# Performance work log

Measured on AMD Instinct MI355X. Metric: run time of the kernel, lower is better.

Reference implementation:

```python
import jax, jax.numpy as jnp
import numpy as np

D_MODEL = 1024
N_HEADS = 16


def setup_inputs() -> dict:
    key = jax.random.key(0)
    ks = jax.random.split(key, 5)
    sigma = (1.0 / D_MODEL) ** 0.5
    return {
        "x": jax.random.normal(ks[0], (4, 2048, D_MODEL), dtype=jnp.float32),
        "W_q": jax.random.normal(ks[1], (D_MODEL, D_MODEL), dtype=jnp.float32) * sigma,
        "W_k": jax.random.normal(ks[2], (D_MODEL, D_MODEL), dtype=jnp.float32) * sigma,
        "W_v": jax.random.normal(ks[3], (D_MODEL, D_MODEL), dtype=jnp.float32) * sigma,
        "W_o": jax.random.normal(ks[4], (D_MODEL, D_MODEL), dtype=jnp.float32) * sigma,
    }


def reference(x, W_q, W_k, W_v, W_o):
    b, s, d = x.shape
    h = N_HEADS
    d_h = d // h
    # Projections: original does einsum('d_out dim, ... dim -> ... d_out') == x @ W.T
    def proj(W):
        y = jnp.einsum('bsd,ed->bse', x, W)
        # ... seq (head d_h) -> ... head seq d_h
        return y.reshape(b, s, h, d_h).transpose(0, 2, 1, 3)
    Q, K, V = proj(W_q), proj(W_k), proj(W_v)
    scale = 1.0 / jnp.sqrt(jnp.asarray(d_h, dtype=x.dtype))
    scores = jnp.einsum('bhqd,bhkd->bhqk', Q, K) * scale  # [b,h,s,s]
    causal = jnp.tril(jnp.ones((s, s), dtype=bool))
    scores = jnp.where(causal, scores, -jnp.inf)
    attn = jax.nn.softmax(scores, axis=-1)
    out = jnp.einsum('bhqk,bhkd->bhqd', attn, V)  # [b,h,s,d_h]
    out = out.transpose(0, 2, 1, 3).reshape(b, s, d)
    # einsum(Temp, W_o, '... dim1, dim dim1 -> ... dim') == Temp @ W_o.T
    return jnp.einsum('bse,de->bsd', out, W_o)
```

## Files before the change

### kernel.cpp

```cpp
#include <hip/hip_runtime.h>

typedef __attribute__((ext_vector_type(8))) short s16x8;
typedef __attribute__((ext_vector_type(4))) short s16x4;
typedef __attribute__((ext_vector_type(4))) float f32x4;
typedef unsigned short u16;
typedef unsigned int u32;
typedef unsigned long long u64;

__device__ __forceinline__ u16 f2bf(float f) {
  unsigned u = __builtin_bit_cast(unsigned, f);
  return (u16)((u + 0x7fffu + ((u >> 16) & 1u)) >> 16);
}

#define QSCALE 0.18033688011112042f

__device__ __forceinline__ void gld16(const u16* g, u16* l) {
  __builtin_amdgcn_global_load_lds(
      (const __attribute__((address_space(1))) void*)g,
      (__attribute__((address_space(3))) void*)l, 16, 0, 0);
}

__device__ __forceinline__ u32 pack_trunc(float a, float b) {
  return __builtin_amdgcn_perm(__builtin_bit_cast(u32, b),
                               __builtin_bit_cast(u32, a), 0x07060302u);
}

__global__ __launch_bounds__(256)
void cvt_all(const float* __restrict__ x,  u16* __restrict__ xb,
             const float* __restrict__ w0, u16* __restrict__ w0b,
             const float* __restrict__ w1, u16* __restrict__ w1b,
             const float* __restrict__ w2, u16* __restrict__ w2b,
             const float* __restrict__ w3, u16* __restrict__ w3b)
{
  int bb = blockIdx.x;
  const float* src; u16* dst; int i;
  if (bb < 4096)      { src = x;  dst = xb;  i = bb * 256 + threadIdx.x; }
  else if (bb < 4608) { src = w0; dst = w0b; i = (bb - 4096) * 256 + threadIdx.x; }
  else if (bb < 5120) { src = w1; dst = w1b; i = (bb - 4608) * 256 + threadIdx.x; }
  else if (bb < 5632) { src = w2; dst = w2b; i = (bb - 5120) * 256 + threadIdx.x; }
  else                { src = w3; dst = w3b; i = (bb - 5632) * 256 + threadIdx.x; }
  f32x4 a = ((const f32x4*)src)[2 * i];
  f32x4 b = ((const f32x4*)src)[2 * i + 1];
  s16x8 pk;
  pk[0] = (short)f2bf(a[0]); pk[1] = (short)f2bf(a[1]);
  pk[2] = (short)f2bf(a[2]); pk[3] = (short)f2bf(a[3]);
  pk[4] = (short)f2bf(b[0]); pk[5] = (short)f2bf(b[1]);
  pk[6] = (short)f2bf(b[2]); pk[7] = (short)f2bf(b[3]);
  ((s16x8*)dst)[i] = pk;
}

template<bool OUT_QKV>
__global__ __launch_bounds__(256)
void gemm97(const u16* __restrict__ A,
            const u16* __restrict__ B0, const u16* __restrict__ B1,
            const u16* __restrict__ B2,
            u16* __restrict__ o0, u16* __restrict__ o1, u16* __restrict__ o2,
            float* __restrict__ oF)
{
  const int by = blockIdx.x;
  const int bx = blockIdx.y;
  const int bz = blockIdx.z;
  const u16* B = (bz == 0) ? B0 : ((bz == 1) ? B1 : B2);
  u16* oQ = (bz == 0) ? o0 : ((bz == 1) ? o1 : o2);

  __shared__ u16 As[128 * 32];
  __shared__ u16 Bs[128 * 32];

  const int tid  = threadIdx.x;
  const int w    = tid >> 6;
  const int lane = tid & 63;
  const int quad = lane >> 4;
  const int l15  = lane & 15;
  const int wm   = (w >> 1) * 64;
  const int wn   = (w & 1) * 64;

  const int arb  = w * 32;
  const int srow = lane >> 2;
  const int scol = (lane & 3) * 8;
  const u16* ga = A + (size_t)(by * 128 + arb + srow) * 1024 + scol;
  const u16* gb = B + (size_t)(bx * 128 + arb + srow) * 1024 + scol;
  u16* la0 = &As[arb * 32];
  u16* la1 = &As[(arb + 16) * 32];
  u16* lb0 = &Bs[arb * 32];
  u16* lb1 = &Bs[(arb + 16) * 32];

  f32x4 acc[4][4];
  #pragma unroll
  for (int i = 0; i < 4; ++i)
    #pragma unroll
    for (int j = 0; j < 4; ++j)
      acc[i][j] = (f32x4){0.f, 0.f, 0.f, 0.f};

  for (int k0 = 0; k0 < 1024; k0 += 32) {
    gld16(ga + k0,               la0);
    gld16(ga + k0 + 16 * 1024,   la1);
    gld16(gb + k0,               lb0);
    gld16(gb + k0 + 16 * 1024,   lb1);
    __syncthreads();

    s16x8 af[4], bf[4];
    #pragma unroll
    for (int i = 0; i < 4; ++i)
      af[i] = *(const s16x8*)&As[(wm + i * 16 + l15) * 32 + quad * 8];
    #pragma unroll
    for (int i = 0; i < 4; ++i)
      bf[i] = *(const s16x8*)&Bs[(wn + i * 16 + l15) * 32 + quad * 8];
    #pragma unroll
    for (int mt = 0; mt < 4; ++mt)
      #pragma unroll
      for (int nt = 0; nt < 4; ++nt)
        acc[mt][nt] = __builtin_amdgcn_mfma_f32_16x16x32_bf16(
            af[mt], bf[nt], acc[mt][nt], 0, 0, 0);
    __syncthreads();
  }

  #pragma unroll
  for (int mt = 0; mt < 4; ++mt)
    #pragma unroll
    for (int nt = 0; nt < 4; ++nt)
      #pragma unroll
      for (int r = 0; r < 4; ++r) {
        const int row = by * 128 + wm + mt * 16 + quad * 4 + r;
        const int col = bx * 128 + wn + nt * 16 + l15;
        float v = acc[mt][nt][r];
        if (OUT_QKV) {
          const int b = row >> 11, s = row & 2047, hh = col >> 6, d = col & 63;
          if (bz == 2) {
            oQ[(size_t)(b * 16 + hh) * 131072 + d * 2048 + s] = f2bf(v);
          } else {
            if (bz == 0) v *= QSCALE;
            oQ[(size_t)(b * 16 + hh) * 131072 + s * 64 + d] = f2bf(v);
          }
        } else {
          oF[(size_t)row * 1024 + col] = v;
        }
      }
}

#define ATTN_STEP(t, Pw, qtt)                                                  \
  do {                                                                         \
    f32x4 S[4];                                                                \
    _Pragma("unroll")                                                          \
    for (int nt = 0; nt < 4; ++nt) {                                           \
      s16x8 b0 = *(const s16x8*)&Ks[(nt * 16 + l15) * 32 + quad * 8];          \
      s16x8 b1 = *(const s16x8*)&Ks[2048 + (nt * 16 + l15) * 32 + quad * 8];   \
      f32x4 z = (f32x4){0.f, 0.f, 0.f, 0.f};                                   \
      z = __builtin_amdgcn_mfma_f32_16x16x32_bf16(aq[t][0], b0, z, 0, 0, 0);   \
      z = __builtin_amdgcn_mfma_f32_16x16x32_bf16(aq[t][1], b1, z, 0, 0, 0);   \
      S[nt] = z;                                                               \
    }                                                                          \
    if (j == (qtt)) {                                                          \
      _Pragma("unroll")                                                        \
      for (int nt = 0; nt < 4; ++nt)                                           \
        _Pragma("unroll")                                                      \
        for (int r = 0; r < 4; ++r) {                                          \
          const int kg = 4 * l15 + nt;                                         \
          const int qg = w * 16 + quad * 4 + r;                                \
          if (kg > qg) S[nt][r] = -1e30f;                                      \
        }                                                                      \
    }                                                                          \
    _Pragma("unroll")                                                          \
    for (int r = 0; r < 4; ++r) {                                              \
      float rm = fmaxf(fmaxf(S[0][r], S[1][r]), fmaxf(S[2][r], S[3][r]));      \
      _Pragma("unroll")                                                        \
      for (int off = 1; off < 16; off <<= 1)                                   \
        rm = fmaxf(rm, __shfl_xor(rm, off, 64));                               \
      const float mold = mi[t][r];                                             \
      const float mnew = fmaxf(mold, rm);                                      \
      const float alpha = __builtin_amdgcn_exp2f(mold - mnew);                 \
      mi[t][r] = mnew;                                                         \
      const float p0 = __builtin_amdgcn_exp2f(S[0][r] - mnew);                 \
      const float p1 = __builtin_amdgcn_exp2f(S[1][r] - mnew);                 \
      const float p2 = __builtin_amdgcn_exp2f(S[2][r] - mnew);                 \
      const float p3 = __builtin_amdgcn_exp2f(S[3][r] - mnew);                 \
      liacc[t][r] *= alpha;                                                    \
      _Pragma("unroll")                                                        \
      for (int dt = 0; dt < 4; ++dt) O[t][dt][r] *= alpha;                     \
      const u64 pk = (u64)pack_trunc(p0, p1) |                                 \
                     ((u64)pack_trunc(p2, p3) << 32);                          \
      *(u64*)&(Pw)[(quad * 4 + r) * 68 + 4 * l15] = pk;                        \
    }                                                                          \
    s16x8 a0 = *(const s16x8*)&(Pw)[l15 * 68 + quad * 8];                      \
    s16x8 a1 = *(const s16x8*)&(Pw)[l15 * 68 + 32 + quad * 8];                 \
    liacc[t] = __builtin_amdgcn_mfma_f32_16x16x32_bf16(a0, ones, liacc[t], 0, 0, 0); \
    liacc[t] = __builtin_amdgcn_mfma_f32_16x16x32_bf16(a1, ones, liacc[t], 0, 0, 0); \
    _Pragma("unroll")                                                          \
    for (int dt = 0; dt < 4; ++dt) {                                           \
      s16x8 b0 = *(const s16x8*)&Vt[(dt * 16 + l15) * 32 + quad * 8];          \
      s16x8 b1 = *(const s16x8*)&Vt[2048 + (dt * 16 + l15) * 32 + quad * 8];   \
      O[t][dt] = __builtin_amdgcn_mfma_f32_16x16x32_bf16(a0, b0, O[t][dt], 0, 0, 0); \
      O[t][dt] = __builtin_amdgcn_mfma_f32_16x16x32_bf16(a1, b1, O[t][dt], 0, 0, 0); \
    }                                                                          \
  } while (0)

__global__ __launch_bounds__(256, 4)
void attn_kernel(const u16* __restrict__ Qg, const u16* __restrict__ Kg,
                 const u16* __restrict__ VTg, u16* __restrict__ out)
{
  const int pi = blockIdx.x;
  const int bh = blockIdx.y;
  const int b = bh >> 4, h = bh & 15;
  const int qt0 = 31 - pi;
  const int qt1 = pi;

  __shared__ u16 Qs[128 * 68];
  __shared__ u16 Ks[2 * 64 * 32];
  __shared__ u16 Vt[2 * 64 * 32];

  const int tid = threadIdx.x;
  const int w = tid >> 6, lane = tid & 63, quad = lane >> 4, l15 = lane & 15;
  const size_t base = (size_t)bh * 131072;

  {
    const int col = (tid & 7) * 8;
    #pragma unroll
    for (int p = 0; p < 4; ++p) {
      const int row = (tid >> 3) + p * 32;
      const int gq = (row < 64) ? (qt0 * 64 + row) : (qt1 * 64 + (row - 64));
      *(s16x8*)&Qs[row * 68 + col] =
          *(const s16x8*)(Qg + base + (size_t)gq * 64 + col);
    }
  }
  __syncthreads();

  s16x8 aq[2][2];
  #pragma unroll
  for (int t = 0; t < 2; ++t)
    #pragma unroll
    for (int ks = 0; ks < 2; ++ks)
      aq[t][ks] = *(const s16x8*)&Qs[(t * 64 + w * 16 + l15) * 68 + ks * 32 + quad * 8];

  u16* Pw0 = &Qs[(w * 16) * 68];
  u16* Pw1 = &Qs[(64 + w * 16) * 68];

  s16x8 ones;
  #pragma unroll
  for (int e = 0; e < 8; ++e) ones[e] = (short)0x3F80;

  f32x4 O[2][4], liacc[2];
  float mi[2][4];
  #pragma unroll
  for (int t = 0; t < 2; ++t) {
    #pragma unroll
    for (int dt = 0; dt < 4; ++dt) O[t][dt] = (f32x4){0.f, 0.f, 0.f, 0.f};
    liacc[t] = (f32x4){0.f, 0.f, 0.f, 0.f};
    #pragma unroll
    for (int r = 0; r < 4; ++r) mi[t][r] = -1e30f;
  }

  const int kkey   = (lane >> 2) * 4 + w;
  const int vd     = w * 16 + (lane >> 2);
  const int chunk  = (lane & 3) * 8;
  const u16* gk = Kg  + base + (size_t)kkey * 64 + chunk;
  const u16* gv = VTg + base + (size_t)vd * 2048 + chunk;
  u16* lk0 = &Ks[w * 16 * 32];
  u16* lk1 = &Ks[2048 + w * 16 * 32];
  u16* lv0 = &Vt[w * 16 * 32];
  u16* lv1 = &Vt[2048 + w * 16 * 32];

  for (int j = 0; j <= qt0; ++j) {
    const size_t koff = (size_t)j * 4096;
    const size_t voff = (size_t)j * 64;
    gld16(gk + koff,      lk0);
    gld16(gk + koff + 32, lk1);
    gld16(gv + voff,      lv0);
    gld16(gv + voff + 32, lv1);
    __syncthreads();

    ATTN_STEP(0, Pw0, qt0);
    if (j <= qt1) ATTN_STEP(1, Pw1, qt1);
    __syncthreads();
  }

  #pragma unroll
  for (int t = 0; t < 2; ++t) {
    const int qtt = t ? qt1 : qt0;
    #pragma unroll
    for (int r = 0; r < 4; ++r) {
      const float inv = __builtin_amdgcn_rcpf(liacc[t][r]);
      const int sq = qtt * 64 + w * 16 + quad * 4 + r;
      #pragma unroll
      for (int dt = 0; dt < 4; ++dt)
        out[(size_t)(b * 2048 + sq) * 1024 + h * 64 + dt * 16 + l15] =
            f2bf(O[t][dt][r] * inv);
    }
  }
}

extern "C" void kernel_launch(void* const* d_in, const int* in_sizes, int n_in,
                              void* d_out, int out_size, void* d_ws, size_t ws_size,
                              hipStream_t stream) {
  (void)in_sizes; (void)n_in; (void)out_size; (void)ws_size;
  const float* x  = (const float*)d_in[0];
  const float* Wq = (const float*)d_in[1];
  const float* Wk = (const float*)d_in[2];
  const float* Wv = (const float*)d_in[3];
  const float* Wo = (const float*)d_in[4];
  float* out = (float*)d_out;

  u16* W16 = (u16*)d_ws;
  u16* xb  = W16;
  u16* AO  = W16;
  u16* Qb  = W16 + 8388608;
  u16* Kb  = W16 + 16777216;
  u16* VT  = W16 + 25165824;
  u16* Wqb = W16 + 33554432;
  u16* Wkb = Wqb + 1048576;
  u16* Wvb = Wkb + 1048576;
  u16* Wob = Wvb + 1048576;

  dim3 blk(256);
  cvt_all<<<dim3(6144), blk, 0, stream>>>(x, xb, Wq, Wqb, Wk, Wkb,
                                          Wv, Wvb, Wo, Wob);
  gemm97<true ><<<dim3(64, 8, 3), blk, 0, stream>>>(
      xb, Wqb, Wkb, Wvb, Qb, Kb, VT, nullptr);
  attn_kernel<<<dim3(16, 64), blk, 0, stream>>>(Qb, Kb, VT, AO);
  gemm97<false><<<dim3(64, 8, 1), blk, 0, stream>>>(
      AO, Wob, Wob, Wob, nullptr, nullptr, nullptr, out);
}
```

Before: 301.8 us.

## Pre-tile K/V in LDS-ready layout and double-buffer K loads in attention

The QKV GEMM epilogue now writes K and V^T directly in the per-64-key tile layout the attention kernel copies into LDS, packing V stores into 64-bit writes. The attention kernel then streams contiguous 8 KB tiles, double-buffers K so the next tile is prefetched during the current step, and overlaps the V load with the QK^T/softmax phase. Q fragments are read straight from global memory and the LDS Q staging is dropped. This removes strided gathers and one barrier per step, at the cost of a tighter sync ordering around the single V buffer and P scratch, which is now shared by both query tiles.

```diff
diff --git a/kernel.cpp b/kernel.cpp
--- a/kernel.cpp
+++ b/kernel.cpp
@@ -117,27 +117,42 @@
   #pragma unroll
   for (int mt = 0; mt < 4; ++mt)
     #pragma unroll
-    for (int nt = 0; nt < 4; ++nt)
-      #pragma unroll
-      for (int r = 0; r < 4; ++r) {
-        const int row = by * 128 + wm + mt * 16 + quad * 4 + r;
-        const int col = bx * 128 + wn + nt * 16 + l15;
-        float v = acc[mt][nt][r];
-        if (OUT_QKV) {
-          const int b = row >> 11, s = row & 2047, hh = col >> 6, d = col & 63;
-          if (bz == 2) {
-            oQ[(size_t)(b * 16 + hh) * 131072 + d * 2048 + s] = f2bf(v);
-          } else {
-            if (bz == 0) v *= QSCALE;
-            oQ[(size_t)(b * 16 + hh) * 131072 + s * 64 + d] = f2bf(v);
+    for (int nt = 0; nt < 4; ++nt) {
+      const int row0 = by * 128 + wm + mt * 16 + quad * 4;
+      const int col  = bx * 128 + wn + nt * 16 + l15;
+      if (OUT_QKV) {
+        const int b = row0 >> 11, s0 = row0 & 2047;
+        const int hh = col >> 6, d = col & 63;
+        const size_t hb = (size_t)(b * 16 + hh) * 131072;
+        if (bz == 2) {
+          const int tile = s0 >> 6, key0 = s0 & 63;
+          const u64 pk = (u64)f2bf(acc[mt][nt][0])
+                       | ((u64)f2bf(acc[mt][nt][1]) << 16)
+                       | ((u64)f2bf(acc[mt][nt][2]) << 32)
+                       | ((u64)f2bf(acc[mt][nt][3]) << 48);
+          *(u64*)&oQ[hb + tile * 4096 + (key0 >> 5) * 2048 + d * 32 + (key0 & 31)] = pk;
+        } else if (bz == 1) {
+          #pragma unroll
+          for (int r = 0; r < 4; ++r) {
+            const int s = s0 + r, tile = s >> 6, key = s & 63;
+            const int slot = (key & 3) * 16 + (key >> 2);
+            oQ[hb + tile * 4096 + (d >> 5) * 2048 + slot * 32 + (d & 31)] =
+                f2bf(acc[mt][nt][r]);
           }
         } else {
-          oF[(size_t)row * 1024 + col] = v;
+          #pragma unroll
+          for (int r = 0; r < 4; ++r)
+            oQ[hb + (size_t)(s0 + r) * 64 + d] = f2bf(acc[mt][nt][r] * QSCALE);
         }
+      } else {
+        #pragma unroll
+        for (int r = 0; r < 4; ++r)
+          oF[(size_t)(row0 + r) * 1024 + col] = acc[mt][nt][r];
       }
-}
-
-#define ATTN_STEP(t, Pw, qtt)                                                  \
+    }
+}
+
+#define ATTN_QKP(t, qtt)                                                       \
   do {                                                                         \
     f32x4 S[4];                                                                \
     _Pragma("unroll")                                                          \
@@ -178,24 +193,28 @@
       for (int dt = 0; dt < 4; ++dt) O[t][dt][r] *= alpha;                     \
       const u64 pk = (u64)pack_trunc(p0, p1) |                                 \
                      ((u64)pack_trunc(p2, p3) << 32);                          \
-      *(u64*)&(Pw)[(quad * 4 + r) * 68 + 4 * l15] = pk;                        \
+      *(u64*)&Pw[(quad * 4 + r) * 68 + 4 * l15] = pk;                          \
     }                                                                          \
-    s16x8 a0 = *(const s16x8*)&(Pw)[l15 * 68 + quad * 8];                      \
-    s16x8 a1 = *(const s16x8*)&(Pw)[l15 * 68 + 32 + quad * 8];                 \
+  } while (0)
+
+#define ATTN_PV(t)                                                             \
+  do {                                                                         \
+    s16x8 a0 = *(const s16x8*)&Pw[l15 * 68 + quad * 8];                        \
+    s16x8 a1 = *(const s16x8*)&Pw[l15 * 68 + 32 + quad * 8];                   \
     liacc[t] = __builtin_amdgcn_mfma_f32_16x16x32_bf16(a0, ones, liacc[t], 0, 0, 0); \
     liacc[t] = __builtin_amdgcn_mfma_f32_16x16x32_bf16(a1, ones, liacc[t], 0, 0, 0); \
     _Pragma("unroll")                                                          \
     for (int dt = 0; dt < 4; ++dt) {                                           \
-      s16x8 b0 = *(const s16x8*)&Vt[(dt * 16 + l15) * 32 + quad * 8];          \
-      s16x8 b1 = *(const s16x8*)&Vt[2048 + (dt * 16 + l15) * 32 + quad * 8];   \
+      s16x8 b0 = *(const s16x8*)&Vbuf[(dt * 16 + l15) * 32 + quad * 8];        \
+      s16x8 b1 = *(const s16x8*)&Vbuf[2048 + (dt * 16 + l15) * 32 + quad * 8]; \
       O[t][dt] = __builtin_amdgcn_mfma_f32_16x16x32_bf16(a0, b0, O[t][dt], 0, 0, 0); \
       O[t][dt] = __builtin_amdgcn_mfma_f32_16x16x32_bf16(a1, b1, O[t][dt], 0, 0, 0); \
     }                                                                          \
   } while (0)
 
 __global__ __launch_bounds__(256, 4)
-void attn_kernel(const u16* __restrict__ Qg, const u16* __restrict__ Kg,
-                 const u16* __restrict__ VTg, u16* __restrict__ out)
+void attn_kernel(const u16* __restrict__ Qg, const u16* __restrict__ Ktg,
+                 const u16* __restrict__ Vtg, u16* __restrict__ out)
 {
   const int pi = blockIdx.x;
   const int bh = blockIdx.y;
@@ -203,35 +222,36 @@
   const int qt0 = 31 - pi;
   const int qt1 = pi;
 
-  __shared__ u16 Qs[128 * 68];
-  __shared__ u16 Ks[2 * 64 * 32];
-  __shared__ u16 Vt[2 * 64 * 32];
+  __shared__ u16 Pl[64 * 68];
+  __shared__ u16 Kbuf[2][4096];
+  __shared__ u16 Vbuf[4096];
 
   const int tid = threadIdx.x;
   const int w = tid >> 6, lane = tid & 63, quad = lane >> 4, l15 = lane & 15;
   const size_t base = (size_t)bh * 131072;
+  const u16* Kt = Ktg + base;
+  const u16* Vt = Vtg + base;
 
   {
-    const int col = (tid & 7) * 8;
-    #pragma unroll
-    for (int p = 0; p < 4; ++p) {
-      const int row = (tid >> 3) + p * 32;
-      const int gq = (row < 64) ? (qt0 * 64 + row) : (qt1 * 64 + (row - 64));
-      *(s16x8*)&Qs[row * 68 + col] =
-          *(const s16x8*)(Qg + base + (size_t)gq * 64 + col);
-    }
-  }
-  __syncthreads();
+    const u16* gk = Kt + w * 1024 + lane * 8;
+    const u16* gv = Vt + w * 1024 + lane * 8;
+    gld16(gk,       &Kbuf[0][w * 1024]);
+    gld16(gk + 512, &Kbuf[0][w * 1024 + 512]);
+    gld16(gv,       &Vbuf[w * 1024]);
+    gld16(gv + 512, &Vbuf[w * 1024 + 512]);
+  }
 
   s16x8 aq[2][2];
   #pragma unroll
-  for (int t = 0; t < 2; ++t)
+  for (int t = 0; t < 2; ++t) {
+    const int qtt = t ? qt1 : qt0;
     #pragma unroll
     for (int ks = 0; ks < 2; ++ks)
-      aq[t][ks] = *(const s16x8*)&Qs[(t * 64 + w * 16 + l15) * 68 + ks * 32 + quad * 8];
-
-  u16* Pw0 = &Qs[(w * 16) * 68];
-  u16* Pw1 = &Qs[(64 + w * 16) * 68];
+      aq[t][ks] = *(const s16x8*)(Qg + base +
+          (size_t)(qtt * 64 + w * 16 + l15) * 64 + ks * 32 + quad * 8);
+  }
+
+  u16* Pw = &Pl[(w * 16) * 68];
 
   s16x8 ones;
   #pragma unroll
@@ -248,28 +268,28 @@
     for (int r = 0; r < 4; ++r) mi[t][r] = -1e30f;
   }
 
-  const int kkey   = (lane >> 2) * 4 + w;
-  const int vd     = w * 16 + (lane >> 2);
-  const int chunk  = (lane & 3) * 8;
-  const u16* gk = Kg  + base + (size_t)kkey * 64 + chunk;
-  const u16* gv = VTg + base + (size_t)vd * 2048 + chunk;
-  u16* lk0 = &Ks[w * 16 * 32];
-  u16* lk1 = &Ks[2048 + w * 16 * 32];
-  u16* lv0 = &Vt[w * 16 * 32];
-  u16* lv1 = &Vt[2048 + w * 16 * 32];
-
   for (int j = 0; j <= qt0; ++j) {
-    const size_t koff = (size_t)j * 4096;
-    const size_t voff = (size_t)j * 64;
-    gld16(gk + koff,      lk0);
-    gld16(gk + koff + 32, lk1);
-    gld16(gv + voff,      lv0);
-    gld16(gv + voff + 32, lv1);
     __syncthreads();
-
-    ATTN_STEP(0, Pw0, qt0);
-    if (j <= qt1) ATTN_STEP(1, Pw1, qt1);
+    const u16* Ks = Kbuf[j & 1];
+    if (j < qt0) {
+      const u16* g = Kt + (size_t)(j + 1) * 4096 + w * 1024 + lane * 8;
+      u16* l = &Kbuf[(j + 1) & 1][w * 1024];
+      gld16(g, l);
+      gld16(g + 512, l + 512);
+    }
+    if (j > 0) {
+      const u16* g = Vt + (size_t)j * 4096 + w * 1024 + lane * 8;
+      gld16(g, &Vbuf[w * 1024]);
+      gld16(g + 512, &Vbuf[w * 1024 + 512]);
+    }
+
+    ATTN_QKP(0, qt0);
     __syncthreads();
+    ATTN_PV(0);
+    if (j <= qt1) {
+      ATTN_QKP(1, qt1);
+      ATTN_PV(1);
+    }
   }
 
   #pragma unroll
@@ -303,7 +323,7 @@
   u16* AO  = W16;
   u16* Qb  = W16 + 8388608;
   u16* Kb  = W16 + 16777216;
-  u16* VT  = W16 + 25165824;
+  u16* Vb  = W16 + 25165824;
   u16* Wqb = W16 + 33554432;
   u16* Wkb = Wqb + 1048576;
   u16* Wvb = Wkb + 1048576;
@@ -313,8 +333,8 @@
   cvt_all<<<dim3(6144), blk, 0, stream>>>(x, xb, Wq, Wqb, Wk, Wkb,
                                           Wv, Wvb, Wo, Wob);
   gemm97<true ><<<dim3(64, 8, 3), blk, 0, stream>>>(
-      xb, Wqb, Wkb, Wvb, Qb, Kb, VT, nullptr);
-  attn_kernel<<<dim3(16, 64), blk, 0, stream>>>(Qb, Kb, VT, AO);
+      xb, Wqb, Wkb, Wvb, Qb, Kb, Vb, nullptr);
+  attn_kernel<<<dim3(16, 64), blk, 0, stream>>>(Qb, Kb, Vb, AO);
   gemm97<false><<<dim3(64, 8, 1), blk, 0, stream>>>(
       AO, Wob, Wob, Wob, nullptr, nullptr, nullptr, out);
 }
```

Measured after the change: 298.3 us. About the same (-1.2%).
